# Performance work log

Hardware: AMD Instinct MI355X
Metric: run time of the kernel (lower is better)

The kernel has to match this reference:

```python
import jax, jax.numpy as jnp
import numpy as np

N_NODES = 50000
N_EDGES = 1600000
HIDDEN = 128
SPATIAL = 3
SCORE_HIDDEN = 128
EPS = 1e-12


def setup_inputs() -> dict:
    key = jax.random.key(0)
    ks = jax.random.split(key, 12)
    s = 0.02
    return {
        "h": jax.random.normal(ks[0], (N_NODES, HIDDEN), dtype=jnp.float32),
        "edge_index": jax.random.randint(ks[1], (2, N_EDGES), 0, N_NODES, dtype=jnp.int64),
        "rel_pos": jax.random.normal(ks[2], (N_EDGES, SPATIAL), dtype=jnp.float32),
        "distance": jax.random.uniform(ks[3], (N_EDGES, 1), dtype=jnp.float32),
        "node_weight": jax.random.uniform(ks[4], (N_NODES,), dtype=jnp.float32),
        "W1": jax.random.normal(ks[5], (2 * HIDDEN + SPATIAL + 1, SCORE_HIDDEN), dtype=jnp.float32) * s,
        "b1": jnp.zeros((SCORE_HIDDEN,), dtype=jnp.float32),
        "W2": jax.random.normal(ks[6], (SCORE_HIDDEN, SCORE_HIDDEN), dtype=jnp.float32) * s,
        "b2": jnp.zeros((SCORE_HIDDEN,), dtype=jnp.float32),
        "W3": jax.random.normal(ks[7], (SCORE_HIDDEN, 1), dtype=jnp.float32) * s,
        "b3": jnp.zeros((1,), dtype=jnp.float32),
        "Wv": jax.random.normal(ks[8], (HIDDEN, HIDDEN), dtype=jnp.float32) * s,
    }


def reference(h, edge_index, rel_pos, distance, node_weight, W1, b1, W2, b2, W3, b3, Wv):
    num_nodes = h.shape[0]
    dst, src = edge_index[0], edge_index[1]
    # per-edge gathered feature: [E, 2*H + spatial + 1]
    edge_feat = jnp.concatenate([h[dst], h[src], rel_pos, distance], axis=-1)
    # 3-layer score MLP -> scalar score per edge
    x = jax.nn.silu(edge_feat @ W1 + b1)
    x = jax.nn.silu(x @ W2 + b2)
    scores = (x @ W3 + b3)[:, 0]  # [E]
    # edge softmax over incoming edges of each dst node
    mx = jax.ops.segment_max(scores, dst, num_segments=num_nodes)  # -inf for empty segments
    exp_scores = jnp.exp(scores - mx[dst])
    den = jax.ops.segment_sum(exp_scores, dst, num_segments=num_nodes)
    alpha = exp_scores / (den[dst] + EPS)
    # value projection, weighted message, scatter-add aggregation
    msg = (h[src] @ Wv) * (alpha * node_weight[src])[:, None]
    out = jax.ops.segment_sum(msg, dst, num_segments=num_nodes)
    return h + out
```

## Files before the change

kernel.cpp:

```cpp
#include <hip/hip_runtime.h>
#include <hip/hip_bf16.h>
#include <cstdint>
#include <cstddef>

#define N_NODES 50000
#define N_EDGES 1600000
#define HID 128
#define PCAT_N 384
#define EPSV 1e-12f

typedef __bf16 bf16_t;
typedef __bf16 bf16x8 __attribute__((ext_vector_type(8)));
typedef float f32x4 __attribute__((ext_vector_type(4)));

__device__ __forceinline__ float bf2f_lo(unsigned u) {
    return __builtin_bit_cast(float, u << 16);
}
__device__ __forceinline__ float bf2f_hi(unsigned u) {
    return __builtin_bit_cast(float, u & 0xFFFF0000u);
}
__device__ __forceinline__ unsigned short f2bf_rne(float x) {
    unsigned u = __builtin_bit_cast(unsigned, x);
    u += 0x7FFFu + ((u >> 16) & 1u);
    return (unsigned short)(u >> 16);
}
__device__ __forceinline__ float silu_f(float x) {
    return x * __builtin_amdgcn_rcpf(1.0f + __expf(-x));
}

__global__ void k_prepw(const float* __restrict__ W1, const float* __restrict__ W2,
                        const float* __restrict__ Wv, bf16_t* __restrict__ wcatT,
                        bf16_t* __restrict__ w2t) {
    int idx = blockIdx.x * blockDim.x + threadIdx.x;
    if (idx < 384 * 128) {
        int n = idx >> 7, k = idx & 127;
        float v;
        if (n < 128)      v = W1[k * 128 + n];
        else if (n < 256) v = W1[(128 + k) * 128 + (n - 128)];
        else              v = Wv[k * 128 + (n - 256)];
        wcatT[idx] = __builtin_bit_cast(bf16_t, f2bf_rne(v));
    } else if (idx < 384 * 128 + 128 * 128) {
        int j = idx - 384 * 128;
        int n = j >> 7, k = j & 127;
        w2t[j] = __builtin_bit_cast(bf16_t, f2bf_rne(W2[k * 128 + n]));
    }
}

__global__ __launch_bounds__(256) void k_nodeproj(
    const float* __restrict__ h, const bf16_t* __restrict__ wcatT,
    const float* __restrict__ nw, bf16_t* __restrict__ pcat) {
    __shared__ bf16_t As[64 * 136];
    int t = threadIdx.x;
    int r0 = blockIdx.x * 64;
    {
        int r = t >> 2, cbase = (t & 3) * 32;
        int gr = r0 + r;
        if (gr >= N_NODES) gr = 0;
        const float* src = h + (size_t)gr * 128 + cbase;
        bf16_t* dst = As + r * 136 + cbase;
#pragma unroll
        for (int i = 0; i < 4; ++i) {
            float4 v0 = *reinterpret_cast<const float4*>(src + i * 8);
            float4 v1 = *reinterpret_cast<const float4*>(src + i * 8 + 4);
            uint4 pk;
            pk.x = (unsigned)f2bf_rne(v0.x) | ((unsigned)f2bf_rne(v0.y) << 16);
            pk.y = (unsigned)f2bf_rne(v0.z) | ((unsigned)f2bf_rne(v0.w) << 16);
            pk.z = (unsigned)f2bf_rne(v1.x) | ((unsigned)f2bf_rne(v1.y) << 16);
            pk.w = (unsigned)f2bf_rne(v1.z) | ((unsigned)f2bf_rne(v1.w) << 16);
            *reinterpret_cast<uint4*>(dst + i * 8) = pk;
        }
    }
    __syncthreads();
    int lane = t & 63, w = t >> 6;
    f32x4 acc[4][6] = {};
#pragma unroll
    for (int kk = 0; kk < 4; ++kk) {
        bf16x8 af[4], bfr[6];
#pragma unroll
        for (int fm = 0; fm < 4; ++fm)
            af[fm] = *reinterpret_cast<const bf16x8*>(
                As + (fm * 16 + (lane & 15)) * 136 + kk * 32 + (lane >> 4) * 8);
#pragma unroll
        for (int fn = 0; fn < 6; ++fn) {
            int n = w * 96 + fn * 16 + (lane & 15);
            bfr[fn] = *reinterpret_cast<const bf16x8*>(
                wcatT + (size_t)n * 128 + kk * 32 + (lane >> 4) * 8);
        }
#pragma unroll
        for (int fm = 0; fm < 4; ++fm)
#pragma unroll
            for (int fn = 0; fn < 6; ++fn)
                acc[fm][fn] = __builtin_amdgcn_mfma_f32_16x16x32_bf16(
                    af[fm], bfr[fn], acc[fm][fn], 0, 0, 0);
    }
#pragma unroll
    for (int fm = 0; fm < 4; ++fm) {
#pragma unroll
        for (int j = 0; j < 4; ++j) {
            int row = r0 + fm * 16 + (lane >> 4) * 4 + j;
            if (row < N_NODES) {
                float nwv = (w >= 2) ? nw[row] : 1.0f;
#pragma unroll
                for (int fn = 0; fn < 6; ++fn) {
                    int colbase = w * 96 + fn * 16;
                    float v = acc[fm][fn][j];
                    if (colbase >= 256) v *= nwv;
                    pcat[(size_t)row * PCAT_N + colbase + (lane & 15)] =
                        __builtin_bit_cast(bf16_t, f2bf_rne(v));
                }
            }
        }
    }
}

__global__ void k_hist(const int* __restrict__ eidx, int* __restrict__ hist) {
    int stride = gridDim.x * blockDim.x;
    for (int e = blockIdx.x * blockDim.x + threadIdx.x; e < N_EDGES; e += stride)
        atomicAdd(&hist[eidx[e]], 1);
}

__global__ __launch_bounds__(1024) void k_scan(const int* __restrict__ hist,
                                               int* __restrict__ row_start,
                                               int* __restrict__ cursor,
                                               float* __restrict__ den) {
    __shared__ int partial[1024];
    int t = threadIdx.x;
    const int C = (N_NODES + 1023) / 1024;
    int base = t * C;
    int sum = 0;
    for (int i = 0; i < C; ++i) {
        int j = base + i;
        if (j < N_NODES) sum += hist[j];
    }
    partial[t] = sum;
    __syncthreads();
    for (int off = 1; off < 1024; off <<= 1) {
        int v = (t >= off) ? partial[t - off] : 0;
        __syncthreads();
        partial[t] += v;
        __syncthreads();
    }
    int run = partial[t] - sum;
    for (int i = 0; i < C; ++i) {
        int j = base + i;
        if (j < N_NODES) {
            row_start[j] = run;
            cursor[j] = run;
            den[j] = 0.0f;
            run += hist[j];
        }
    }
    if (t == 1023) row_start[N_NODES] = partial[1023];
}

__global__ void k_scatter(const int* __restrict__ eidx,
                          const float* __restrict__ rel_pos,
                          const float* __restrict__ dist,
                          int* __restrict__ cursor,
                          uint4* __restrict__ recs) {
    int stride = gridDim.x * blockDim.x;
    for (int e = blockIdx.x * blockDim.x + threadIdx.x; e < N_EDGES; e += stride) {
        int d = eidx[e];
        int sv = eidx[N_EDGES + e];
        float r0 = rel_pos[(size_t)e * 3];
        float r1 = rel_pos[(size_t)e * 3 + 1];
        float r2 = rel_pos[(size_t)e * 3 + 2];
        float dd = dist[e];
        uint4 rec;
        rec.x = (unsigned)f2bf_rne(r0) | ((unsigned)f2bf_rne(r1) << 16);
        rec.y = (unsigned)f2bf_rne(r2) | ((unsigned)f2bf_rne(dd) << 16);
        rec.z = (unsigned)d;
        rec.w = (unsigned)sv;
        int pos = atomicAdd(&cursor[d], 1);
        recs[pos] = rec;
    }
}

__global__ __launch_bounds__(256, 6) void k_fused(
    const bf16_t* __restrict__ pcat, const bf16_t* __restrict__ w2t,
    const uint4* __restrict__ recs, const float* __restrict__ W1,
    const float* __restrict__ b1, const float* __restrict__ b2,
    const float* __restrict__ W3, const float* __restrict__ b3,
    float* __restrict__ den, float* __restrict__ outp) {
    __shared__ bf16_t Ax[64 * 136];
    __shared__ int s_dst[64];
    __shared__ int s_src[64];
    __shared__ float4 s_rp[64];
    __shared__ float s_sc[64];
    __shared__ int s_runstart[65];
    __shared__ int s_runnode[64];
    __shared__ int s_nruns;

    int t = threadIdx.x;
    int e0 = blockIdx.x * 64;
    if (t < 64) {
        uint4 rec = recs[e0 + t];
        s_dst[t] = (int)rec.z;
        s_src[t] = (int)rec.w;
        s_rp[t] = make_float4(bf2f_lo(rec.x), bf2f_hi(rec.x),
                              bf2f_lo(rec.y), bf2f_hi(rec.y));
        s_sc[t] = b3[0];
    }
    int lane = t & 63, w = t >> 6;
    int c0 = 2 * lane;
    float wA0 = W1[256 * 128 + c0], wA1 = W1[257 * 128 + c0];
    float wA2 = W1[258 * 128 + c0], wA3 = W1[259 * 128 + c0];
    float bA = b1[c0];
    float wB0 = W1[256 * 128 + c0 + 1], wB1 = W1[257 * 128 + c0 + 1];
    float wB2 = W1[258 * 128 + c0 + 1], wB3 = W1[259 * 128 + c0 + 1];
    float bB = b1[c0 + 1];
    __syncthreads();

    if (t < 64) {
        bool flag = (t == 0) || (s_dst[t] != s_dst[t - 1]);
        unsigned long long mask = __ballot((int)flag);
        int rid = (int)__popcll(mask & ((2ull << t) - 1)) - 1;
        if (flag) {
            s_runstart[rid] = t;
            s_runnode[rid] = s_dst[t];
        }
        if (t == 0) {
            int nr = (int)__popcll(mask);
            s_nruns = nr;
            s_runstart[nr] = 64;
        }
    }

#pragma unroll 4
    for (int i = 0; i < 16; ++i) {
        int e = w * 16 + i;
        int dn = s_dst[e], sn = s_src[e];
        float4 rp = s_rp[e];
        unsigned pa = *reinterpret_cast<const unsigned*>(pcat + (size_t)dn * PCAT_N + c0);
        unsigned pb = *reinterpret_cast<const unsigned*>(pcat + (size_t)sn * PCAT_N + 128 + c0);
        float x0 = bf2f_lo(pa) + bf2f_lo(pb) +
                   rp.x * wA0 + rp.y * wA1 + rp.z * wA2 + rp.w * wA3 + bA;
        float x1 = bf2f_hi(pa) + bf2f_hi(pb) +
                   rp.x * wB0 + rp.y * wB1 + rp.z * wB2 + rp.w * wB3 + bB;
        float y0 = silu_f(x0), y1 = silu_f(x1);
        unsigned pk = (unsigned)f2bf_rne(y0) | ((unsigned)f2bf_rne(y1) << 16);
        *reinterpret_cast<unsigned*>(Ax + e * 136 + c0) = pk;
    }
    __syncthreads();

    f32x4 acc[4][2] = {};
#pragma unroll
    for (int kk = 0; kk < 4; ++kk) {
        bf16x8 af[4], bfr[2];
#pragma unroll
        for (int fn = 0; fn < 2; ++fn) {
            int n = w * 32 + fn * 16 + (lane & 15);
            bfr[fn] = *reinterpret_cast<const bf16x8*>(
                w2t + (size_t)n * 128 + kk * 32 + (lane >> 4) * 8);
        }
#pragma unroll
        for (int fm = 0; fm < 4; ++fm)
            af[fm] = *reinterpret_cast<const bf16x8*>(
                Ax + (fm * 16 + (lane & 15)) * 136 + kk * 32 + (lane >> 4) * 8);
#pragma unroll
        for (int fm = 0; fm < 4; ++fm)
#pragma unroll
            for (int fn = 0; fn < 2; ++fn)
                acc[fm][fn] = __builtin_amdgcn_mfma_f32_16x16x32_bf16(
                    af[fm], bfr[fn], acc[fm][fn], 0, 0, 0);
    }

    float w3v[2], b2v[2];
#pragma unroll
    for (int fn = 0; fn < 2; ++fn) {
        int n = w * 32 + fn * 16 + (lane & 15);
        w3v[fn] = W3[n];
        b2v[fn] = b2[n];
    }
#pragma unroll
    for (int fm = 0; fm < 4; ++fm) {
        float pj[4] = {0.f, 0.f, 0.f, 0.f};
#pragma unroll
        for (int fn = 0; fn < 2; ++fn) {
#pragma unroll
            for (int j = 0; j < 4; ++j)
                pj[j] += silu_f(acc[fm][fn][j] + b2v[fn]) * w3v[fn];
        }
#pragma unroll
        for (int j = 0; j < 4; ++j) {
            float v = pj[j];
            v += __shfl_xor(v, 1);
            v += __shfl_xor(v, 2);
            v += __shfl_xor(v, 4);
            v += __shfl_xor(v, 8);
            if ((lane & 15) == 0)
                atomicAdd(&s_sc[fm * 16 + (lane >> 4) * 4 + j], v);
        }
    }
    __syncthreads();

    int nruns = s_nruns;
    for (int r = w; r < nruns; r += 4) {
        int node = s_runnode[r];
        int j0 = s_runstart[r], j1 = s_runstart[r + 1];
        float a0 = 0.f, a1 = 0.f, ad = 0.f;
        for (int j = j0; j < j1; ++j) {
            float c = __expf(s_sc[j]);
            int sv = s_src[j];
            unsigned hv = *reinterpret_cast<const unsigned*>(
                pcat + (size_t)sv * PCAT_N + 256 + c0);
            a0 += c * bf2f_lo(hv);
            a1 += c * bf2f_hi(hv);
            ad += c;
        }
        atomicAdd(&outp[(size_t)node * 128 + c0], a0);
        atomicAdd(&outp[(size_t)node * 128 + c0 + 1], a1);
        if (lane == 0) atomicAdd(&den[node], ad);
    }
}

__global__ __launch_bounds__(256) void k_norm(const float* __restrict__ h,
                                              const float* __restrict__ den,
                                              float* __restrict__ outp) {
    int idx = blockIdx.x * 256 + threadIdx.x;
    int node = idx >> 6;
    float inv = __builtin_amdgcn_rcpf(den[node] + EPSV);
    float2 n2 = *reinterpret_cast<const float2*>(outp + (size_t)idx * 2);
    float2 h2 = *reinterpret_cast<const float2*>(h + (size_t)idx * 2);
    float2 res;
    res.x = h2.x + n2.x * inv;
    res.y = h2.y + n2.y * inv;
    *reinterpret_cast<float2*>(outp + (size_t)idx * 2) = res;
}

extern "C" void kernel_launch(void* const* d_in, const int* in_sizes, int n_in,
                              void* d_out, int out_size, void* d_ws, size_t ws_size,
                              hipStream_t stream) {
    const float* h       = (const float*)d_in[0];
    const int*   eidx    = (const int*)d_in[1];
    const float* rel_pos = (const float*)d_in[2];
    const float* dist    = (const float*)d_in[3];
    const float* nw      = (const float*)d_in[4];
    const float* W1      = (const float*)d_in[5];
    const float* b1      = (const float*)d_in[6];
    const float* W2      = (const float*)d_in[7];
    const float* b2      = (const float*)d_in[8];
    const float* W3      = (const float*)d_in[9];
    const float* b3      = (const float*)d_in[10];
    const float* Wv      = (const float*)d_in[11];
    float* out = (float*)d_out;

    char* p = (char*)d_ws;
    auto carve = [&](size_t bytes) {
        char* r = p;
        p += (bytes + 255) & ~(size_t)255;
        return r;
    };
    bf16_t* pcat    = (bf16_t*)carve((size_t)N_NODES * PCAT_N * 2);
    bf16_t* wcatT   = (bf16_t*)carve(384 * 128 * 2);
    bf16_t* w2t     = (bf16_t*)carve(128 * 128 * 2);
    uint4* recs     = (uint4*)carve((size_t)N_EDGES * 16);
    int* hist       = (int*)carve((size_t)N_NODES * 4);
    int* row_start  = (int*)carve((size_t)(N_NODES + 1) * 4);
    int* cursor     = (int*)carve((size_t)N_NODES * 4);
    float* den      = (float*)carve((size_t)N_NODES * 4);

    hipMemsetAsync(hist, 0, (size_t)N_NODES * 4, stream);
    hipMemsetAsync(out, 0, (size_t)N_NODES * HID * 4, stream);
    k_prepw<<<256, 256, 0, stream>>>(W1, W2, Wv, wcatT, w2t);
    k_nodeproj<<<(N_NODES + 63) / 64, 256, 0, stream>>>(h, wcatT, nw, pcat);
    k_hist<<<2048, 256, 0, stream>>>(eidx, hist);
    k_scan<<<1, 1024, 0, stream>>>(hist, row_start, cursor, den);
    k_scatter<<<2048, 256, 0, stream>>>(eidx, rel_pos, dist, cursor, recs);
    k_fused<<<N_EDGES / 64, 256, 0, stream>>>(pcat, w2t, recs, W1, b1, b2,
                                              W3, b3, den, out);
    k_norm<<<(N_NODES * HID / 2) / 256, 256, 0, stream>>>(h, den, out);
}
```

Before: 783.2 us.

## Compact edge records to 8 bytes with fp8 geometry, fuse histogram, batch aggregation

Edge records shrink from 16 to 8 bytes. The dst and src indices are packed as 16-bit values, and rel_pos and distance are stored in a custom fp8 (e4m3-like) encoding. The histogram pass moves into the tail of the node projection kernel, and the unused row_start output is dropped. The per-block run detection is replaced by each wave processing a fixed 16-edge slice, with batched gathers of the value rows and on-the-fly segment flushes via atomics. Launch bounds on the fused kernel are relaxed from 6 to 5 blocks per CU. Together these aim to cut record traffic and launch count and to raise memory-level parallelism, at the cost of lower precision on the geometric features and possibly more atomics per node.

```diff
diff --git a/kernel.cpp b/kernel.cpp
--- a/kernel.cpp
+++ b/kernel.cpp
@@ -26,6 +26,22 @@
 }
 __device__ __forceinline__ float silu_f(float x) {
     return x * __builtin_amdgcn_rcpf(1.0f + __expf(-x));
+}
+__device__ __forceinline__ unsigned enc_fp8(float x) {
+    unsigned u = __builtin_bit_cast(unsigned, x);
+    unsigned s = (u >> 24) & 0x80u;
+    unsigned mag = u & 0x7FFFFFFFu;
+    if (mag > 0x43E00000u) mag = 0x43E00000u;
+    if (mag < 0x3C800000u) return s;
+    unsigned r = mag + 0x7FFFFu + ((mag >> 20) & 1u);
+    unsigned e = (r >> 23) - 120u;
+    unsigned m = (r >> 20) & 7u;
+    return s | (e << 3) | m;
+}
+__device__ __forceinline__ float dec_fp8(unsigned c) {
+    unsigned e = (c >> 3) & 0xFu;
+    unsigned u = ((c & 0x80u) << 24) | ((e + 120u) << 23) | ((c & 7u) << 20);
+    return e ? __builtin_bit_cast(float, u) : 0.0f;
 }
 
 __global__ void k_prepw(const float* __restrict__ W1, const float* __restrict__ W2,
@@ -48,7 +64,8 @@
 
 __global__ __launch_bounds__(256) void k_nodeproj(
     const float* __restrict__ h, const bf16_t* __restrict__ wcatT,
-    const float* __restrict__ nw, bf16_t* __restrict__ pcat) {
+    const float* __restrict__ nw, bf16_t* __restrict__ pcat,
+    const int* __restrict__ eidx, int* __restrict__ hist) {
     __shared__ bf16_t As[64 * 136];
     int t = threadIdx.x;
     int r0 = blockIdx.x * 64;
@@ -111,16 +128,12 @@
             }
         }
     }
-}
-
-__global__ void k_hist(const int* __restrict__ eidx, int* __restrict__ hist) {
-    int stride = gridDim.x * blockDim.x;
-    for (int e = blockIdx.x * blockDim.x + threadIdx.x; e < N_EDGES; e += stride)
+    int stride = gridDim.x * 256;
+    for (int e = blockIdx.x * 256 + t; e < N_EDGES; e += stride)
         atomicAdd(&hist[eidx[e]], 1);
 }
 
 __global__ __launch_bounds__(1024) void k_scan(const int* __restrict__ hist,
-                                               int* __restrict__ row_start,
                                                int* __restrict__ cursor,
                                                float* __restrict__ den) {
     __shared__ int partial[1024];
@@ -144,20 +157,18 @@
     for (int i = 0; i < C; ++i) {
         int j = base + i;
         if (j < N_NODES) {
-            row_start[j] = run;
             cursor[j] = run;
             den[j] = 0.0f;
             run += hist[j];
         }
     }
-    if (t == 1023) row_start[N_NODES] = partial[1023];
 }
 
 __global__ void k_scatter(const int* __restrict__ eidx,
                           const float* __restrict__ rel_pos,
                           const float* __restrict__ dist,
                           int* __restrict__ cursor,
-                          uint4* __restrict__ recs) {
+                          uint2* __restrict__ recs) {
     int stride = gridDim.x * blockDim.x;
     for (int e = blockIdx.x * blockDim.x + threadIdx.x; e < N_EDGES; e += stride) {
         int d = eidx[e];
@@ -166,19 +177,18 @@
         float r1 = rel_pos[(size_t)e * 3 + 1];
         float r2 = rel_pos[(size_t)e * 3 + 2];
         float dd = dist[e];
-        uint4 rec;
-        rec.x = (unsigned)f2bf_rne(r0) | ((unsigned)f2bf_rne(r1) << 16);
-        rec.y = (unsigned)f2bf_rne(r2) | ((unsigned)f2bf_rne(dd) << 16);
-        rec.z = (unsigned)d;
-        rec.w = (unsigned)sv;
+        uint2 rec;
+        rec.x = ((unsigned)d << 16) | (unsigned)sv;
+        rec.y = enc_fp8(r0) | (enc_fp8(r1) << 8) | (enc_fp8(r2) << 16) |
+                (enc_fp8(dd) << 24);
         int pos = atomicAdd(&cursor[d], 1);
         recs[pos] = rec;
     }
 }
 
-__global__ __launch_bounds__(256, 6) void k_fused(
+__global__ __launch_bounds__(256, 5) void k_fused(
     const bf16_t* __restrict__ pcat, const bf16_t* __restrict__ w2t,
-    const uint4* __restrict__ recs, const float* __restrict__ W1,
+    const uint2* __restrict__ recs, const float* __restrict__ W1,
     const float* __restrict__ b1, const float* __restrict__ b2,
     const float* __restrict__ W3, const float* __restrict__ b3,
     float* __restrict__ den, float* __restrict__ outp) {
@@ -187,18 +197,15 @@
     __shared__ int s_src[64];
     __shared__ float4 s_rp[64];
     __shared__ float s_sc[64];
-    __shared__ int s_runstart[65];
-    __shared__ int s_runnode[64];
-    __shared__ int s_nruns;
 
     int t = threadIdx.x;
     int e0 = blockIdx.x * 64;
     if (t < 64) {
-        uint4 rec = recs[e0 + t];
-        s_dst[t] = (int)rec.z;
-        s_src[t] = (int)rec.w;
-        s_rp[t] = make_float4(bf2f_lo(rec.x), bf2f_hi(rec.x),
-                              bf2f_lo(rec.y), bf2f_hi(rec.y));
+        uint2 rec = recs[e0 + t];
+        s_dst[t] = (int)(rec.x >> 16);
+        s_src[t] = (int)(rec.x & 0xFFFFu);
+        s_rp[t] = make_float4(dec_fp8(rec.y & 0xFFu), dec_fp8((rec.y >> 8) & 0xFFu),
+                              dec_fp8((rec.y >> 16) & 0xFFu), dec_fp8(rec.y >> 24));
         s_sc[t] = b3[0];
     }
     int lane = t & 63, w = t >> 6;
@@ -210,21 +217,6 @@
     float wB2 = W1[258 * 128 + c0 + 1], wB3 = W1[259 * 128 + c0 + 1];
     float bB = b1[c0 + 1];
     __syncthreads();
-
-    if (t < 64) {
-        bool flag = (t == 0) || (s_dst[t] != s_dst[t - 1]);
-        unsigned long long mask = __ballot((int)flag);
-        int rid = (int)__popcll(mask & ((2ull << t) - 1)) - 1;
-        if (flag) {
-            s_runstart[rid] = t;
-            s_runnode[rid] = s_dst[t];
-        }
-        if (t == 0) {
-            int nr = (int)__popcll(mask);
-            s_nruns = nr;
-            s_runstart[nr] = 64;
-        }
-    }
 
 #pragma unroll 4
     for (int i = 0; i < 16; ++i) {
@@ -294,23 +286,40 @@
     }
     __syncthreads();
 
-    int nruns = s_nruns;
-    for (int r = w; r < nruns; r += 4) {
-        int node = s_runnode[r];
-        int j0 = s_runstart[r], j1 = s_runstart[r + 1];
+    {
+        int jb = w * 16;
         float a0 = 0.f, a1 = 0.f, ad = 0.f;
-        for (int j = j0; j < j1; ++j) {
-            float c = __expf(s_sc[j]);
-            int sv = s_src[j];
-            unsigned hv = *reinterpret_cast<const unsigned*>(
-                pcat + (size_t)sv * PCAT_N + 256 + c0);
-            a0 += c * bf2f_lo(hv);
-            a1 += c * bf2f_hi(hv);
-            ad += c;
-        }
-        atomicAdd(&outp[(size_t)node * 128 + c0], a0);
-        atomicAdd(&outp[(size_t)node * 128 + c0 + 1], a1);
-        if (lane == 0) atomicAdd(&den[node], ad);
+        int cur = s_dst[jb];
+        for (int half = 0; half < 2; ++half) {
+            float cv[8], flo[8], fhi[8];
+#pragma unroll
+            for (int i = 0; i < 8; ++i) {
+                int j = jb + half * 8 + i;
+                cv[i] = __expf(s_sc[j]);
+                unsigned hv = *reinterpret_cast<const unsigned*>(
+                    pcat + (size_t)s_src[j] * PCAT_N + 256 + c0);
+                flo[i] = bf2f_lo(hv);
+                fhi[i] = bf2f_hi(hv);
+            }
+#pragma unroll
+            for (int i = 0; i < 8; ++i) {
+                int j = jb + half * 8 + i;
+                int d = s_dst[j];
+                if (d != cur) {
+                    atomicAdd(&outp[(size_t)cur * 128 + c0], a0);
+                    atomicAdd(&outp[(size_t)cur * 128 + c0 + 1], a1);
+                    if (lane == 0) atomicAdd(&den[cur], ad);
+                    a0 = a1 = ad = 0.f;
+                    cur = d;
+                }
+                a0 += cv[i] * flo[i];
+                a1 += cv[i] * fhi[i];
+                ad += cv[i];
+            }
+        }
+        atomicAdd(&outp[(size_t)cur * 128 + c0], a0);
+        atomicAdd(&outp[(size_t)cur * 128 + c0 + 1], a1);
+        if (lane == 0) atomicAdd(&den[cur], ad);
     }
 }
 
@@ -354,18 +363,17 @@
     bf16_t* pcat    = (bf16_t*)carve((size_t)N_NODES * PCAT_N * 2);
     bf16_t* wcatT   = (bf16_t*)carve(384 * 128 * 2);
     bf16_t* w2t     = (bf16_t*)carve(128 * 128 * 2);
-    uint4* recs     = (uint4*)carve((size_t)N_EDGES * 16);
+    uint2* recs     = (uint2*)carve((size_t)N_EDGES * 8);
     int* hist       = (int*)carve((size_t)N_NODES * 4);
-    int* row_start  = (int*)carve((size_t)(N_NODES + 1) * 4);
     int* cursor     = (int*)carve((size_t)N_NODES * 4);
     float* den      = (float*)carve((size_t)N_NODES * 4);
 
     hipMemsetAsync(hist, 0, (size_t)N_NODES * 4, stream);
     hipMemsetAsync(out, 0, (size_t)N_NODES * HID * 4, stream);
     k_prepw<<<256, 256, 0, stream>>>(W1, W2, Wv, wcatT, w2t);
-    k_nodeproj<<<(N_NODES + 63) / 64, 256, 0, stream>>>(h, wcatT, nw, pcat);
-    k_hist<<<2048, 256, 0, stream>>>(eidx, hist);
-    k_scan<<<1, 1024, 0, stream>>>(hist, row_start, cursor, den);
+    k_nodeproj<<<(N_NODES + 63) / 64, 256, 0, stream>>>(h, wcatT, nw, pcat,
+                                                        eidx, hist);
+    k_scan<<<1, 1024, 0, stream>>>(hist, cursor, den);
     k_scatter<<<2048, 256, 0, stream>>>(eidx, rel_pos, dist, cursor, recs);
     k_fused<<<N_EDGES / 64, 256, 0, stream>>>(pcat, w2t, recs, W1, b1, b2,
                                               W3, b3, den, out);
```

Measured after the change: 706.7 us. 9.8% less time.
